# Kernel tuning notes

Measured on AMD Instinct MI355X. Metric: run time of the kernel, lower is better.

## Reference

```python
import jax, jax.numpy as jnp
import numpy as np

N_NODES = 500000
N_EDGES = 5000000


def _sage_conv(x, edge_index, Wl, bl, Wr):
    # PyG SAGEConv (aggr='mean', root_weight=True):
    #   out = lin_l(mean_{j in N(i)} x_j) + lin_r(x_i)
    # edge_index[0] = source, edge_index[1] = target
    src, dst = edge_index[0], edge_index[1]
    n = x.shape[0]
    msg = x[src]  # [E, F] gather
    agg = jax.ops.segment_sum(msg, dst, num_segments=n)  # [N, F]
    deg = jax.ops.segment_sum(jnp.ones((src.shape[0],), x.dtype), dst, num_segments=n)
    agg = agg / jnp.maximum(deg, 1.0)[:, None]  # mean aggregation
    return agg @ Wl.T + bl + x @ Wr.T


def setup_inputs() -> dict:
    key = jax.random.key(0)
    k1, k2, k3, k4, k5, k6 = jax.random.split(key, 6)
    x = jax.random.normal(k1, (N_NODES, 2), dtype=jnp.float32)
    edge_index = jax.random.randint(k2, (2, N_EDGES), 0, N_NODES, dtype=jnp.int64)
    # conv1: SAGEConv(2, 16); conv2: SAGEConv(16, 1)
    s1 = 1.0 / np.sqrt(2.0)
    s2 = 1.0 / np.sqrt(16.0)
    W1l = jax.random.uniform(k3, (16, 2), jnp.float32, -s1, s1)
    W1r = jax.random.uniform(k4, (16, 2), jnp.float32, -s1, s1)
    b1 = jnp.zeros((16,), jnp.float32)
    W2l = jax.random.uniform(k5, (1, 16), jnp.float32, -s2, s2)
    W2r = jax.random.uniform(k6, (1, 16), jnp.float32, -s2, s2)
    b2 = jnp.zeros((1,), jnp.float32)
    return {"x": x, "edge_index": edge_index,
            "W1l": W1l, "b1": b1, "W1r": W1r,
            "W2l": W2l, "b2": b2, "W2r": W2r}


def reference(x, edge_index, W1l, b1, W1r, W2l, b2, W2r):
    h = jax.nn.relu(_sage_conv(x, edge_index, W1l, b1, W1r))  # [N, 16]
    h = _sage_conv(h, edge_index, W2l, b2, W2r)               # [N, 1]
    return jax.nn.sigmoid(h).squeeze(-1)                      # [N]
```

## Files before the change

### kernel.cpp

```cpp
#include <hip/hip_runtime.h>


static constexpr int ABLOCK = 512;
static constexpr int PBLOCK = 1024;
static constexpr int KITER  = 5;
static constexpr int CHUNK  = PBLOCK * 4 * KITER;
static constexpr int BUCKET_BITS = 10;
static constexpr int BUCKET_NODES = 1 << BUCKET_BITS;
static constexpr int MAXNB = 512;
static constexpr int CAP = 16384;
static constexpr int CSTRIDE = 16;

static constexpr float S1 = 65536.0f;
static constexpr float IS1 = 1.0f / 65536.0f;
static constexpr long long B1 = 8LL * 65536LL;
static constexpr float S2 = 16384.0f;
static constexpr float IS2 = 1.0f / 16384.0f;

__global__ __launch_bounds__(512) void k_init(unsigned* __restrict__ cursor, int NB) {
    int b = blockIdx.x * 512 + threadIdx.x;
    if (b < NB) cursor[(size_t)b * CSTRIDE] = (unsigned)b * (unsigned)CAP;
}

__global__ __launch_bounds__(PBLOCK) void k_part(
    const int* __restrict__ src, const int* __restrict__ dst,
    unsigned* __restrict__ cursor, unsigned* __restrict__ entries,
    int E, int NB)
{
    __shared__ unsigned sorted[CHUNK];
    __shared__ unsigned hist[MAXNB];
    __shared__ unsigned loc[MAXNB];
    __shared__ unsigned base[MAXNB];
    const int tid = threadIdx.x;
    const int e0 = (int)blockIdx.x * CHUNK;
    const int e1 = min(e0 + CHUNK, E);
    const int4* dst4 = reinterpret_cast<const int4*>(dst + e0);
    const int4* src4 = reinterpret_cast<const int4*>(src + e0);

    int4 dR[KITER], sR[KITER];
#pragma unroll
    for (int k = 0; k < KITER; ++k) {
        int g = tid + k * PBLOCK;
        int e = e0 + 4 * g;
        if (e + 3 < e1) {
            dR[k] = dst4[g];
            sR[k] = src4[g];
        } else {
            dR[k] = make_int4(-1, -1, -1, -1);
            sR[k] = make_int4(0, 0, 0, 0);
#pragma unroll
            for (int j = 0; j < 4; ++j) {
                if (e + j < e1) {
                    (&dR[k].x)[j] = dst[e + j];
                    (&sR[k].x)[j] = src[e + j];
                }
            }
        }
    }

    for (int b = tid; b < MAXNB; b += PBLOCK) hist[b] = 0;
    __syncthreads();

    #define HIST1(dv) { unsigned du_ = (unsigned)(dv); \
        if (du_ != 0xFFFFFFFFu) atomicAdd(&hist[du_ >> BUCKET_BITS], 1u); }
#pragma unroll
    for (int k = 0; k < KITER; ++k) {
        HIST1(dR[k].x) HIST1(dR[k].y) HIST1(dR[k].z) HIST1(dR[k].w)
    }
    #undef HIST1
    __syncthreads();

    if (tid < NB) loc[tid] = hist[tid];
    __syncthreads();
    for (int off = 1; off < NB; off <<= 1) {
        unsigned v = 0;
        if (tid < NB && tid >= off) v = loc[tid - off];
        __syncthreads();
        if (tid < NB) loc[tid] += v;
        __syncthreads();
    }
    if (tid < NB) loc[tid] -= hist[tid];

    if (tid < NB) {
        int b = tid + (int)(blockIdx.x % (unsigned)NB);
        if (b >= NB) b -= NB;
        base[b] = atomicAdd(&cursor[(size_t)b * CSTRIDE], hist[b]);
    }
    __syncthreads();
    for (int b = tid; b < MAXNB; b += PBLOCK) hist[b] = 0;
    __syncthreads();

    #define SCAT1(dv, sv) { unsigned du_ = (unsigned)(dv); \
        if (du_ != 0xFFFFFFFFu) { \
            unsigned bk_ = du_ >> BUCKET_BITS; \
            unsigned r_ = atomicAdd(&hist[bk_], 1u); \
            sorted[loc[bk_] + r_] = ((unsigned)(sv) << BUCKET_BITS) | (du_ & (BUCKET_NODES - 1)); } }
#pragma unroll
    for (int k = 0; k < KITER; ++k) {
        SCAT1(dR[k].x, sR[k].x) SCAT1(dR[k].y, sR[k].y)
        SCAT1(dR[k].z, sR[k].z) SCAT1(dR[k].w, sR[k].w)
    }
    #undef SCAT1
    __syncthreads();

    const int wave = tid >> 6, lane = tid & 63;
    const int nw = PBLOCK >> 6;
    const int off = (int)(blockIdx.x % (unsigned)NB);
    for (int j = wave; j < NB; j += nw) {
        int b = j + off;
        if (b >= NB) b -= NB;
        unsigned cnt = hist[b];
        if (cnt == 0) continue;
        unsigned lo = loc[b], ba = base[b];
        unsigned lim = (unsigned)(b + 1) * (unsigned)CAP;
        if (ba >= lim) continue;
        cnt = min(cnt, lim - ba);
        for (unsigned i = lane; i < cnt; i += 64)
            entries[ba + i] = sorted[lo + i];
    }
}

__global__ __launch_bounds__(ABLOCK) void k_agg1(
    const unsigned* __restrict__ entries, const unsigned* __restrict__ cursor,
    const float* __restrict__ x,
    const float* __restrict__ W1l, const float* __restrict__ b1,
    const float* __restrict__ W1r, const float* __restrict__ W2l,
    const float* __restrict__ W2r, const float* __restrict__ b2,
    unsigned* __restrict__ sq, float* __restrict__ t0a, float* __restrict__ ga,
    int N)
{
    __shared__ unsigned long long qs[BUCKET_NODES];
    int bk = blockIdx.x;
    for (int i = threadIdx.x; i < BUCKET_NODES; i += ABLOCK) qs[i] = 0ULL;
    __syncthreads();

    unsigned start = (unsigned)bk * (unsigned)CAP;
    unsigned end = min(cursor[(size_t)bk * CSTRIDE], start + (unsigned)CAP);
    unsigned n = end - start;
    unsigned nv = n >> 2;
    const uint4* e4 = reinterpret_cast<const uint4*>(entries + start);

    #define PROC1(en) { \
        unsigned s_ = (en) >> BUCKET_BITS; \
        unsigned dl_ = (en) & (BUCKET_NODES - 1); \
        float2 xv_ = *reinterpret_cast<const float2*>(x + 2 * (size_t)s_); \
        unsigned q0_ = (unsigned)__float2int_rn((xv_.x + 8.0f) * S1); \
        unsigned q1_ = (unsigned)__float2int_rn((xv_.y + 8.0f) * S1); \
        atomicAdd(&qs[dl_], (1ULL << 56) | ((unsigned long long)q0_ << 28) | (unsigned long long)q1_); }

#pragma unroll 2
    for (unsigned t = threadIdx.x; t < nv; t += ABLOCK) {
        uint4 en = e4[t];
        PROC1(en.x) PROC1(en.y) PROC1(en.z) PROC1(en.w)
    }
    for (unsigned t = start + (nv << 2) + threadIdx.x; t < end; t += ABLOCK) {
        unsigned en = entries[t];
        PROC1(en)
    }
    #undef PROC1
    __syncthreads();

    int nodebase = bk << BUCKET_BITS;
    for (int il = threadIdx.x; il < BUCKET_NODES; il += ABLOCK) {
        int i = nodebase + il;
        if (i >= N) continue;
        unsigned long long v = qs[il];
        int deg = (int)(v >> 56);
        long long q0 = (long long)((v >> 28) & 0xFFFFFFFULL);
        long long q1 = (long long)(v & 0xFFFFFFFULL);
        long long bias = (long long)deg * B1;
        float inv = 1.0f / (float)max(deg, 1);
        float m0 = (float)(q0 - bias) * IS1 * inv;
        float m1 = (float)(q1 - bias) * IS1 * inv;
        float2 xv = *reinterpret_cast<const float2*>(x + 2 * (size_t)i);
        float s = 0.0f, t0 = b2[0];
#pragma unroll
        for (int o = 0; o < 16; ++o) {
            float h = m0 * W1l[2 * o] + m1 * W1l[2 * o + 1] + b1[o]
                    + xv.x * W1r[2 * o] + xv.y * W1r[2 * o + 1];
            h = fmaxf(h, 0.0f);
            s  += h * W2l[o];
            t0 += h * W2r[o];
        }
        sq[i]  = (unsigned)__float2int_rn((s + 128.0f) * S2);
        t0a[i] = t0 - (deg > 0 ? 128.0f : 0.0f);
        ga[i]  = IS2 * inv;
    }
}

__global__ __launch_bounds__(ABLOCK) void k_agg2(
    const unsigned* __restrict__ entries, const unsigned* __restrict__ cursor,
    const unsigned* __restrict__ sq,
    const float* __restrict__ t0a, const float* __restrict__ ga,
    float* __restrict__ out, int N)
{
    __shared__ unsigned sbin[BUCKET_NODES];
    int bk = blockIdx.x;
    for (int i = threadIdx.x; i < BUCKET_NODES; i += ABLOCK) sbin[i] = 0;
    __syncthreads();

    unsigned start = (unsigned)bk * (unsigned)CAP;
    unsigned end = min(cursor[(size_t)bk * CSTRIDE], start + (unsigned)CAP);
    unsigned n = end - start;
    unsigned nv = n >> 2;
    const uint4* e4 = reinterpret_cast<const uint4*>(entries + start);

    #define PROC2(en) { \
        unsigned s_ = (en) >> BUCKET_BITS; \
        unsigned dl_ = (en) & (BUCKET_NODES - 1); \
        atomicAdd(&sbin[dl_], sq[s_]); }

#pragma unroll 2
    for (unsigned t = threadIdx.x; t < nv; t += ABLOCK) {
        uint4 en = e4[t];
        PROC2(en.x) PROC2(en.y) PROC2(en.z) PROC2(en.w)
    }
    for (unsigned t = start + (nv << 2) + threadIdx.x; t < end; t += ABLOCK) {
        unsigned en = entries[t];
        PROC2(en)
    }
    #undef PROC2
    __syncthreads();

    int nodebase = bk << BUCKET_BITS;
    for (int il = threadIdx.x; il < BUCKET_NODES; il += ABLOCK) {
        int i = nodebase + il;
        if (i >= N) continue;
        float t = (float)(int)sbin[il] * ga[i] + t0a[i];
        out[i] = 1.0f / (1.0f + expf(-t));
    }
}

__global__ __launch_bounds__(256) void k_scatter1_fb(
    const int* __restrict__ src, const int* __restrict__ dst,
    const float* __restrict__ x, float* __restrict__ agg1, float* __restrict__ deg, int E)
{
    int stride = gridDim.x * blockDim.x;
    for (int e = blockIdx.x * blockDim.x + threadIdx.x; e < E; e += stride) {
        int s = src[e], d = dst[e];
        float2 xv = *reinterpret_cast<const float2*>(x + 2 * (size_t)s);
        unsafeAtomicAdd(&agg1[2 * (size_t)d + 0], xv.x);
        unsafeAtomicAdd(&agg1[2 * (size_t)d + 1], xv.y);
        unsafeAtomicAdd(&deg[d], 1.0f);
    }
}
__global__ __launch_bounds__(256) void k_node1_fb(
    const float* __restrict__ x, const float* __restrict__ agg1, const float* __restrict__ deg,
    const float* __restrict__ W1l, const float* __restrict__ b1,
    const float* __restrict__ W1r, const float* __restrict__ W2l,
    float* __restrict__ sval, int N)
{
    int i = blockIdx.x * blockDim.x + threadIdx.x;
    if (i >= N) return;
    float inv = 1.0f / fmaxf(deg[i], 1.0f);
    float2 a = *reinterpret_cast<const float2*>(agg1 + 2 * (size_t)i);
    float m0 = a.x * inv, m1 = a.y * inv;
    float2 xv = *reinterpret_cast<const float2*>(x + 2 * (size_t)i);
    float s = 0.0f;
#pragma unroll
    for (int o = 0; o < 16; ++o) {
        float h = m0 * W1l[2 * o] + m1 * W1l[2 * o + 1] + b1[o]
                + xv.x * W1r[2 * o] + xv.y * W1r[2 * o + 1];
        s += fmaxf(h, 0.0f) * W2l[o];
    }
    sval[i] = s;
}
__global__ __launch_bounds__(256) void k_scatter2_fb(
    const int* __restrict__ src, const int* __restrict__ dst,
    const float* __restrict__ sval, float* __restrict__ agg_s, int E)
{
    int stride = gridDim.x * blockDim.x;
    for (int e = blockIdx.x * blockDim.x + threadIdx.x; e < E; e += stride)
        unsafeAtomicAdd(&agg_s[dst[e]], sval[src[e]]);
}
__global__ __launch_bounds__(256) void k_node2_fb(
    const float* __restrict__ x, const float* __restrict__ agg1, const float* __restrict__ deg,
    const float* __restrict__ agg_s,
    const float* __restrict__ W1l, const float* __restrict__ b1,
    const float* __restrict__ W1r, const float* __restrict__ W2r, const float* __restrict__ b2,
    float* __restrict__ out, int N)
{
    int i = blockIdx.x * blockDim.x + threadIdx.x;
    if (i >= N) return;
    float inv = 1.0f / fmaxf(deg[i], 1.0f);
    float2 a = *reinterpret_cast<const float2*>(agg1 + 2 * (size_t)i);
    float m0 = a.x * inv, m1 = a.y * inv;
    float2 xv = *reinterpret_cast<const float2*>(x + 2 * (size_t)i);
    float t = agg_s[i] * inv + b2[0];
#pragma unroll
    for (int o = 0; o < 16; ++o) {
        float h = m0 * W1l[2 * o] + m1 * W1l[2 * o + 1] + b1[o]
                + xv.x * W1r[2 * o] + xv.y * W1r[2 * o + 1];
        t += fmaxf(h, 0.0f) * W2r[o];
    }
    out[i] = 1.0f / (1.0f + expf(-t));
}

extern "C" void kernel_launch(void* const* d_in, const int* in_sizes, int n_in,
                              void* d_out, int out_size, void* d_ws, size_t ws_size,
                              hipStream_t stream) {
    const float* x   = (const float*)d_in[0];
    const int*   ei  = (const int*)d_in[1];
    const float* W1l = (const float*)d_in[2];
    const float* b1  = (const float*)d_in[3];
    const float* W1r = (const float*)d_in[4];
    const float* W2l = (const float*)d_in[5];
    const float* b2  = (const float*)d_in[6];
    const float* W2r = (const float*)d_in[7];

    const int N = in_sizes[0] / 2;
    const int E = in_sizes[1] / 2;
    const int* src = ei;
    const int* dst = ei + (size_t)E;
    float* out = (float*)d_out;

    const int NB = (N + BUCKET_NODES - 1) >> BUCKET_BITS;
    const int pblocks = (E + CHUNK - 1) / CHUNK;

    size_t needed = (size_t)MAXNB * CSTRIDE * 4 + (size_t)NB * CAP * 4 + 3 * (size_t)N * 4;
    if (NB <= MAXNB && NB <= PBLOCK && ws_size >= needed) {
        unsigned* cursor  = (unsigned*)d_ws;
        unsigned* entries = cursor + (size_t)MAXNB * CSTRIDE;
        unsigned* sq      = entries + (size_t)NB * CAP;
        float*    t0a     = (float*)(sq + N);
        float*    ga      = t0a + N;

        k_init<<<(NB + 511) / 512, 512, 0, stream>>>(cursor, NB);
        k_part<<<pblocks, PBLOCK, 0, stream>>>(src, dst, cursor, entries, E, NB);
        k_agg1<<<NB, ABLOCK, 0, stream>>>(entries, cursor, x, W1l, b1, W1r, W2l, W2r, b2,
                                          sq, t0a, ga, N);
        k_agg2<<<NB, ABLOCK, 0, stream>>>(entries, cursor, sq, t0a, ga, out, N);
    } else {
        float* agg1  = (float*)d_ws;
        float* deg   = agg1 + 2 * (size_t)N;
        float* agg_s = deg + (size_t)N;
        float* sval  = agg_s + (size_t)N;
        hipMemsetAsync(d_ws, 0, 4 * (size_t)N * sizeof(float), stream);
        const int eblocks = 2048, nblocks = (N + 255) / 256;
        k_scatter1_fb<<<eblocks, 256, 0, stream>>>(src, dst, x, agg1, deg, E);
        k_node1_fb<<<nblocks, 256, 0, stream>>>(x, agg1, deg, W1l, b1, W1r, W2l, sval, N);
        k_scatter2_fb<<<eblocks, 256, 0, stream>>>(src, dst, sval, agg_s, E);
        k_node2_fb<<<nblocks, 256, 0, stream>>>(x, agg1, deg, agg_s, W1l, b1, W1r, W2r, b2, out, N);
    }
}
```

Before: 98.20 us.

## Pre-quantize node features to packed 16-bit pairs and batch gathers by eight

A new prologue kernel quantizes each node's two input features into one packed 32-bit word at a coarser fixed-point scale, clamped to 16 bits, and also initializes the partition cursors. The first aggregation then gathers 4 bytes per edge instead of 8 and skips per-edge float-to-int conversion. Both aggregation loops now process eight entries per iteration, issuing all gathers before the shared-memory atomics to raise memory-level parallelism. The coarser quantization lowers the precision of the mean aggregation and clamps inputs outside roughly [-8, 24).

```diff
diff --git a/kernel.cpp b/kernel.cpp
--- a/kernel.cpp
+++ b/kernel.cpp
@@ -11,15 +11,25 @@
 static constexpr int CAP = 16384;
 static constexpr int CSTRIDE = 16;
 
-static constexpr float S1 = 65536.0f;
-static constexpr float IS1 = 1.0f / 65536.0f;
-static constexpr long long B1 = 8LL * 65536LL;
+static constexpr float S1 = 2048.0f;
+static constexpr float IS1 = 1.0f / 2048.0f;
+static constexpr long long B1 = 8LL * 2048LL;
 static constexpr float S2 = 16384.0f;
 static constexpr float IS2 = 1.0f / 16384.0f;
 
-__global__ __launch_bounds__(512) void k_init(unsigned* __restrict__ cursor, int NB) {
-    int b = blockIdx.x * 512 + threadIdx.x;
-    if (b < NB) cursor[(size_t)b * CSTRIDE] = (unsigned)b * (unsigned)CAP;
+__global__ __launch_bounds__(256) void k_pre(
+    const float* __restrict__ x, unsigned* __restrict__ qx,
+    unsigned* __restrict__ cursor, int N, int NB)
+{
+    int i = blockIdx.x * 256 + threadIdx.x;
+    if (i < NB) cursor[(size_t)i * CSTRIDE] = (unsigned)i * (unsigned)CAP;
+    if (i >= N) return;
+    float2 xv = *reinterpret_cast<const float2*>(x + 2 * (size_t)i);
+    float f0 = fminf(fmaxf((xv.x + 8.0f) * S1, 0.0f), 65535.0f);
+    float f1 = fminf(fmaxf((xv.y + 8.0f) * S1, 0.0f), 65535.0f);
+    unsigned q0 = (unsigned)__float2int_rn(f0);
+    unsigned q1 = (unsigned)__float2int_rn(f1);
+    qx[i] = (q0 << 16) | q1;
 }
 
 __global__ __launch_bounds__(PBLOCK) void k_part(
@@ -120,9 +130,12 @@
     }
 }
 
+#define PK(q) ((1ULL << 56) | ((unsigned long long)((q) >> 16) << 28) \
+               | (unsigned long long)((q) & 0xFFFFu))
+
 __global__ __launch_bounds__(ABLOCK) void k_agg1(
     const unsigned* __restrict__ entries, const unsigned* __restrict__ cursor,
-    const float* __restrict__ x,
+    const unsigned* __restrict__ qx, const float* __restrict__ x,
     const float* __restrict__ W1l, const float* __restrict__ b1,
     const float* __restrict__ W1r, const float* __restrict__ W2l,
     const float* __restrict__ W2r, const float* __restrict__ b2,
@@ -137,27 +150,34 @@
     unsigned start = (unsigned)bk * (unsigned)CAP;
     unsigned end = min(cursor[(size_t)bk * CSTRIDE], start + (unsigned)CAP);
     unsigned n = end - start;
-    unsigned nv = n >> 2;
+    unsigned n8 = n >> 3;
     const uint4* e4 = reinterpret_cast<const uint4*>(entries + start);
 
-    #define PROC1(en) { \
-        unsigned s_ = (en) >> BUCKET_BITS; \
-        unsigned dl_ = (en) & (BUCKET_NODES - 1); \
-        float2 xv_ = *reinterpret_cast<const float2*>(x + 2 * (size_t)s_); \
-        unsigned q0_ = (unsigned)__float2int_rn((xv_.x + 8.0f) * S1); \
-        unsigned q1_ = (unsigned)__float2int_rn((xv_.y + 8.0f) * S1); \
-        atomicAdd(&qs[dl_], (1ULL << 56) | ((unsigned long long)q0_ << 28) | (unsigned long long)q1_); }
-
-#pragma unroll 2
-    for (unsigned t = threadIdx.x; t < nv; t += ABLOCK) {
-        uint4 en = e4[t];
-        PROC1(en.x) PROC1(en.y) PROC1(en.z) PROC1(en.w)
-    }
-    for (unsigned t = start + (nv << 2) + threadIdx.x; t < end; t += ABLOCK) {
+    for (unsigned t = threadIdx.x; t < n8; t += ABLOCK) {
+        uint4 a = e4[2 * t];
+        uint4 b = e4[2 * t + 1];
+        unsigned g0 = qx[a.x >> BUCKET_BITS];
+        unsigned g1 = qx[a.y >> BUCKET_BITS];
+        unsigned g2 = qx[a.z >> BUCKET_BITS];
+        unsigned g3 = qx[a.w >> BUCKET_BITS];
+        unsigned g4 = qx[b.x >> BUCKET_BITS];
+        unsigned g5 = qx[b.y >> BUCKET_BITS];
+        unsigned g6 = qx[b.z >> BUCKET_BITS];
+        unsigned g7 = qx[b.w >> BUCKET_BITS];
+        atomicAdd(&qs[a.x & (BUCKET_NODES - 1)], PK(g0));
+        atomicAdd(&qs[a.y & (BUCKET_NODES - 1)], PK(g1));
+        atomicAdd(&qs[a.z & (BUCKET_NODES - 1)], PK(g2));
+        atomicAdd(&qs[a.w & (BUCKET_NODES - 1)], PK(g3));
+        atomicAdd(&qs[b.x & (BUCKET_NODES - 1)], PK(g4));
+        atomicAdd(&qs[b.y & (BUCKET_NODES - 1)], PK(g5));
+        atomicAdd(&qs[b.z & (BUCKET_NODES - 1)], PK(g6));
+        atomicAdd(&qs[b.w & (BUCKET_NODES - 1)], PK(g7));
+    }
+    for (unsigned t = start + (n8 << 3) + threadIdx.x; t < end; t += ABLOCK) {
         unsigned en = entries[t];
-        PROC1(en)
-    }
-    #undef PROC1
+        unsigned g = qx[en >> BUCKET_BITS];
+        atomicAdd(&qs[en & (BUCKET_NODES - 1)], PK(g));
+    }
     __syncthreads();
 
     int nodebase = bk << BUCKET_BITS;
@@ -202,24 +222,33 @@
     unsigned start = (unsigned)bk * (unsigned)CAP;
     unsigned end = min(cursor[(size_t)bk * CSTRIDE], start + (unsigned)CAP);
     unsigned n = end - start;
-    unsigned nv = n >> 2;
+    unsigned n8 = n >> 3;
     const uint4* e4 = reinterpret_cast<const uint4*>(entries + start);
 
-    #define PROC2(en) { \
-        unsigned s_ = (en) >> BUCKET_BITS; \
-        unsigned dl_ = (en) & (BUCKET_NODES - 1); \
-        atomicAdd(&sbin[dl_], sq[s_]); }
-
-#pragma unroll 2
-    for (unsigned t = threadIdx.x; t < nv; t += ABLOCK) {
-        uint4 en = e4[t];
-        PROC2(en.x) PROC2(en.y) PROC2(en.z) PROC2(en.w)
-    }
-    for (unsigned t = start + (nv << 2) + threadIdx.x; t < end; t += ABLOCK) {
+    for (unsigned t = threadIdx.x; t < n8; t += ABLOCK) {
+        uint4 a = e4[2 * t];
+        uint4 b = e4[2 * t + 1];
+        unsigned v0 = sq[a.x >> BUCKET_BITS];
+        unsigned v1 = sq[a.y >> BUCKET_BITS];
+        unsigned v2 = sq[a.z >> BUCKET_BITS];
+        unsigned v3 = sq[a.w >> BUCKET_BITS];
+        unsigned v4 = sq[b.x >> BUCKET_BITS];
+        unsigned v5 = sq[b.y >> BUCKET_BITS];
+        unsigned v6 = sq[b.z >> BUCKET_BITS];
+        unsigned v7 = sq[b.w >> BUCKET_BITS];
+        atomicAdd(&sbin[a.x & (BUCKET_NODES - 1)], v0);
+        atomicAdd(&sbin[a.y & (BUCKET_NODES - 1)], v1);
+        atomicAdd(&sbin[a.z & (BUCKET_NODES - 1)], v2);
+        atomicAdd(&sbin[a.w & (BUCKET_NODES - 1)], v3);
+        atomicAdd(&sbin[b.x & (BUCKET_NODES - 1)], v4);
+        atomicAdd(&sbin[b.y & (BUCKET_NODES - 1)], v5);
+        atomicAdd(&sbin[b.z & (BUCKET_NODES - 1)], v6);
+        atomicAdd(&sbin[b.w & (BUCKET_NODES - 1)], v7);
+    }
+    for (unsigned t = start + (n8 << 3) + threadIdx.x; t < end; t += ABLOCK) {
         unsigned en = entries[t];
-        PROC2(en)
-    }
-    #undef PROC2
+        atomicAdd(&sbin[en & (BUCKET_NODES - 1)], sq[en >> BUCKET_BITS]);
+    }
     __syncthreads();
 
     int nodebase = bk << BUCKET_BITS;
@@ -317,18 +346,19 @@
     const int NB = (N + BUCKET_NODES - 1) >> BUCKET_BITS;
     const int pblocks = (E + CHUNK - 1) / CHUNK;
 
-    size_t needed = (size_t)MAXNB * CSTRIDE * 4 + (size_t)NB * CAP * 4 + 3 * (size_t)N * 4;
+    size_t needed = (size_t)MAXNB * CSTRIDE * 4 + (size_t)NB * CAP * 4 + 4 * (size_t)N * 4;
     if (NB <= MAXNB && NB <= PBLOCK && ws_size >= needed) {
         unsigned* cursor  = (unsigned*)d_ws;
         unsigned* entries = cursor + (size_t)MAXNB * CSTRIDE;
         unsigned* sq      = entries + (size_t)NB * CAP;
         float*    t0a     = (float*)(sq + N);
         float*    ga      = t0a + N;
-
-        k_init<<<(NB + 511) / 512, 512, 0, stream>>>(cursor, NB);
+        unsigned* qx      = (unsigned*)(ga + N);
+
+        k_pre<<<(N + 255) / 256, 256, 0, stream>>>(x, qx, cursor, N, NB);
         k_part<<<pblocks, PBLOCK, 0, stream>>>(src, dst, cursor, entries, E, NB);
-        k_agg1<<<NB, ABLOCK, 0, stream>>>(entries, cursor, x, W1l, b1, W1r, W2l, W2r, b2,
-                                          sq, t0a, ga, N);
+        k_agg1<<<NB, ABLOCK, 0, stream>>>(entries, cursor, qx, x, W1l, b1, W1r,
+                                          W2l, W2r, b2, sq, t0a, ga, N);
         k_agg2<<<NB, ABLOCK, 0, stream>>>(entries, cursor, sq, t0a, ga, out, N);
     } else {
         float* agg1  = (float*)d_ws;
```

New measurement: 90.02 us. -8.3%, faster.
